# Optimization experiments

Measured on AMD Instinct MI355X. Metric: run time of the kernel, lower is better.

The kernel has to match this reference:

```python
import jax, jax.numpy as jnp
import numpy as np

KSIZE = 3; STRIDE = 1; RATE = 2; FUSE_K = 3; SCALE = 10.0; EPS = 1e-4
B, C, RH, RW = 2, 128, 80, 80  # raw (full-res) feature shape


def setup_inputs() -> dict:
    key = jax.random.key(0)
    ks = jax.random.split(key, 5)
    shp = (B, C, RH, RW)
    names = ["left", "right", "mid", "raw_left", "raw_right"]
    return {n: jax.random.normal(k, shp, dtype=jnp.float32) for n, k in zip(names, ks)}


def _same_pads(H, W, k, s):
    oh, ow = -(-H // s), -(-W // s)
    ph = max(0, (oh - 1) * s + k - H)
    pw = max(0, (ow - 1) * s + k - W)
    return ((ph // 2, ph - ph // 2), (pw // 2, pw - pw // 2))


def extract_patches(x, k, s):
    # torch extract_image_patches with 'same' padding -> (b, L, c, k, k)
    b, c, H, W = x.shape
    pads = _same_pads(H, W, k, s)
    p = jax.lax.conv_general_dilated_patches(x, (k, k), (s, s), pads)  # (b, c*k*k, oh, ow)
    oh, ow = p.shape[2], p.shape[3]
    p = p.reshape(b, c, k, k, oh * ow)  # feature dim is channel-major (c, k, k), like torch unfold
    return p.transpose(0, 4, 1, 2, 3)


def _fuse(s, Hl, Wl, Hm, Wm):
    # diagonal fuse-conv: conv of (b,1,L,P) score image with eye(k), twice with transposes
    b = s.shape[0]
    k = FUSE_K
    eye = jnp.eye(k, dtype=s.dtype).reshape(1, 1, k, k)
    pad = ((k // 2, k // 2), (k // 2, k // 2))
    conv = lambda x: jax.lax.conv_general_dilated(x, eye, (1, 1), pad)
    x = conv(s.reshape(b, 1, Hl * Wl, Hm * Wm))
    x = x.reshape(b, Hl, Wl, Hm, Wm).transpose(0, 2, 1, 4, 3).reshape(b, 1, Wl * Hl, Wm * Hm)
    x = conv(x)
    x = x.reshape(b, Wl, Hl, Wm, Hm).transpose(0, 2, 1, 4, 3)  # (b, Hl, Wl, Hm, Wm)
    return x.reshape(b, Hl * Wl, Hm, Wm)


def _deconv_one(attn, patches):
    # torch conv_transpose2d(attn, patches, stride=RATE, padding=1):
    # conv with lhs dilation RATE, spatially-flipped kernel, padding k-1-1
    kk = patches.shape[-1]
    rhs = jnp.flip(patches, (-2, -1)).transpose(1, 0, 2, 3)  # (C, L, kk, kk)
    p = kk - 1 - 1
    out = jax.lax.conv_general_dilated(attn[None], rhs, (1, 1), ((p, p), (p, p)),
                                       lhs_dilation=(RATE, RATE),
                                       dimension_numbers=('NCHW', 'OIHW', 'NCHW'))
    return out[0]


def _forward(left, right, mid, raw_left, raw_right):
    kernel = 2 * RATE
    rawp_l = extract_patches(raw_left, kernel, RATE * STRIDE)   # (B, L, C, 4, 4)
    rawp_r = extract_patches(raw_right, kernel, RATE * STRIDE)
    # nearest downsample by rate
    l = left[:, :, ::RATE, ::RATE]
    r = right[:, :, ::RATE, ::RATE]
    m = mid[:, :, ::RATE, ::RATE]
    Hl, Wl = l.shape[2], l.shape[3]
    Hm, Wm = m.shape[2], m.shape[3]
    lp = extract_patches(l, KSIZE, STRIDE)   # (B, L, C, 3, 3)
    rp = extract_patches(r, KSIZE, STRIDE)
    mp = extract_patches(m, KSIZE, STRIDE)   # (B, P, C, 3, 3); conv2d(same-padded xi, w) == patch dot

    def norm(p):
        # torch: sqrt(reduce_sum(p^2 + eps)) -- eps added elementwise before the sum
        return p / jnp.sqrt(jnp.sum(p * p + EPS, axis=(2, 3, 4), keepdims=True))

    sl = jnp.einsum('bqcij,bpcij->bqp', norm(lp), mp).reshape(-1, Hl * Wl, Hm, Wm)
    sr = jnp.einsum('bqcij,bpcij->bqp', norm(rp), mp).reshape(-1, Hl * Wl, Hm, Wm)
    sl = _fuse(sl, Hl, Wl, Hm, Wm)
    sr = _fuse(sr, Hl, Wl, Hm, Wm)
    al = jax.nn.softmax(sl * SCALE, axis=1)
    ar = jax.nn.softmax(sr * SCALE, axis=1)
    y_l = jax.vmap(_deconv_one)(al, rawp_l) / 4.0   # (B, C, RH, RW)
    y_r = jax.vmap(_deconv_one)(ar, rawp_r) / 4.0
    # cos_function_weight: cosine blending ramp along width (1 at left edge -> 0 at right edge)
    w = 0.5 * (1.0 + jnp.cos(jnp.pi * jnp.arange(RW, dtype=y_l.dtype) / (RW - 1)))
    w = w.reshape(1, 1, 1, RW)
    return w * y_l + jnp.flip(w, 3) * y_r


def reference(left, right, mid, raw_left, raw_right):
    return _forward(left, right, mid, raw_left, raw_right)
```

## Files before the change

kernel.cpp:

```cpp
#include <hip/hip_runtime.h>
#include <hip/hip_bf16.h>

typedef __hip_bfloat16 bf16;
typedef __attribute__((ext_vector_type(8))) short short8;
typedef __attribute__((ext_vector_type(4))) float f32x4;
typedef float f32x4u __attribute__((ext_vector_type(4), aligned(4)));
typedef unsigned short ushort_t;

#define PI_F 3.14159265358979323846f
#define GPAD_Z 3111696L

#define GLOAD_LDS16(gp, lp)                                                    \
  __builtin_amdgcn_global_load_lds(                                            \
      (const __attribute__((address_space(1))) unsigned int*)(gp),             \
      (__attribute__((address_space(3))) unsigned int*)(lp), 16, 0, 0)

__global__ __launch_bounds__(128) void prep_pt(const float* __restrict__ left,
                                               const float* __restrict__ right,
                                               const float* __restrict__ mid,
                                               bf16* __restrict__ PTe,
                                               bf16* __restrict__ MTe,
                                               float* __restrict__ SQ) {
  int q = blockIdx.x;
  int y = blockIdx.y;
  int c = threadIdx.x;
  int qi = q / 40, qj = q - qi * 40;
  const float* src;
  bf16* dst;
  int b;
  bool aside = (y < 4);
  if (aside) {
    b = y & 1;
    src = (y < 2) ? left : right;
    dst = PTe + (long)y * 1664 * 384;
  } else {
    b = y - 4;
    src = mid;
    dst = MTe + (long)(y - 4) * 1664 * 384;
  }
  float v = src[(((long)b * 128 + c) * 80 + 2 * qi) * 80 + 2 * qj];
  bf16 hi = __float2bfloat16(v);
  bf16 lo = __float2bfloat16(v - __bfloat162float(hi));
  if (aside) {
    dst[(long)q * 384 + c] = hi;
    dst[(long)q * 384 + 128 + c] = lo;
    dst[(long)q * 384 + 256 + c] = hi;
  } else {
    dst[(long)q * 384 + c] = hi;
    dst[(long)q * 384 + 128 + c] = hi;
    dst[(long)q * 384 + 256 + c] = lo;
  }
  if (aside) {
    __shared__ float red[128];
    red[c] = v * v;
    __syncthreads();
    for (int s = 64; s > 0; s >>= 1) {
      if (c < s) red[c] += red[c + s];
      __syncthreads();
    }
    if (c == 0) SQ[y * 1600 + q] = red[0];
  }
}

__global__ void invn_kernel(const float* __restrict__ SQ, float* __restrict__ INV) {
  int idx = blockIdx.x * 256 + threadIdx.x;
  if (idx >= 6400) return;
  int z = idx / 1600, q = idx - z * 1600;
  int qi = q / 40, qj = q - qi * 40;
  float s = 0.1152f;
  #pragma unroll
  for (int di = -1; di <= 1; ++di)
    #pragma unroll
    for (int dj = -1; dj <= 1; ++dj) {
      int a = qi + di, b = qj + dj;
      if (a >= 0 && a < 40 && b >= 0 && b < 40) s += SQ[z * 1600 + a * 40 + b];
    }
  INV[idx] = rsqrtf(s);
}

__global__ __launch_bounds__(256) void padzero_kernel(float* __restrict__ Gp) {
  int row = blockIdx.x;
  int z = blockIdx.y;
  float* R = Gp + (long)z * GPAD_Z + (long)row * 1764;
  int r42 = row % 42;
  if (r42 == 0 || r42 == 41) {
    for (int c = threadIdx.x; c < 1764; c += 256) R[c] = 0.f;
  } else {
    for (int i = threadIdx.x; i < 84; i += 256) {
      int c = (i >> 1) * 42 + ((i & 1) ? 41 : 0);
      R[c] = 0.f;
    }
  }
}

__global__ __launch_bounds__(256) void gemm_nt(const bf16* __restrict__ A,
                                               const bf16* __restrict__ B,
                                               float* __restrict__ C,
                                               int M, int N, int K,
                                               long Az, long Bz, long Cz,
                                               int bmod, int cpad) {
  int z = blockIdx.z;
  A += (long)z * Az;
  B += (long)(bmod ? (z & 1) : z) * Bz;
  C += (long)z * Cz;
  __shared__ bf16 As[128 * 32];
  __shared__ bf16 Bs[128 * 32];
  int lane = threadIdx.x & 63;
  int w = threadIdx.x >> 6;
  int mb = blockIdx.x * 128;
  int nb = blockIdx.y * 128;
  int lr = lane >> 2;
  int gb = (lane & 3) ^ ((lane >> 3) & 3);
  int lm = lane & 15;
  int swz = (lm >> 1) & 3;
  int kb = lane >> 4;
  int pos = (kb ^ swz) * 8;
  int warow = (w >> 1) * 64;
  int wbrow = (w & 1) * 64;
  f32x4 acc[4][4];
  #pragma unroll
  for (int i = 0; i < 4; ++i)
    #pragma unroll
    for (int j = 0; j < 4; ++j) {
      f32x4 zv = {0.f, 0.f, 0.f, 0.f};
      acc[i][j] = zv;
    }
  for (int k0 = 0; k0 < K; k0 += 32) {
    __syncthreads();
    #pragma unroll
    for (int t = 0; t < 2; ++t) {
      int r = (w * 2 + t) * 16 + lr;
      GLOAD_LDS16(A + (long)(mb + r) * K + k0 + gb * 8, As + (w * 2 + t) * 512);
      GLOAD_LDS16(B + (long)(nb + r) * K + k0 + gb * 8, Bs + (w * 2 + t) * 512);
    }
    __syncthreads();
    short8 af[4], bfr[4];
    #pragma unroll
    for (int i = 0; i < 4; ++i) {
      af[i]  = *reinterpret_cast<const short8*>(As + (warow + i * 16 + lm) * 32 + pos);
      bfr[i] = *reinterpret_cast<const short8*>(Bs + (wbrow + i * 16 + lm) * 32 + pos);
    }
    #pragma unroll
    for (int i = 0; i < 4; ++i)
      #pragma unroll
      for (int j = 0; j < 4; ++j)
        acc[i][j] = __builtin_amdgcn_mfma_f32_16x16x32_bf16(af[i], bfr[j], acc[i][j], 0, 0, 0);
  }
  int m0 = mb + warow;
  int n0 = nb + wbrow;
  int col = lane & 15;
  int r0 = (lane >> 4) * 4;
  #pragma unroll
  for (int i = 0; i < 4; ++i)
    #pragma unroll
    for (int j = 0; j < 4; ++j) {
      int n = n0 + j * 16 + col;
      if (n < N) {
        int nc = cpad ? ((n / 40) * 42 + (n - (n / 40) * 40) + 43) : n;
        #pragma unroll
        for (int r = 0; r < 4; ++r) {
          int m = m0 + i * 16 + r0 + r;
          if (m < M) {
            long mr = cpad ? ((long)((m / 40) * 42 + (m - (m / 40) * 40) + 43) * 1764)
                           : ((long)m * N);
            C[mr + nc] = acc[i][j][r];
          }
        }
      }
    }
}

#define BAR() __builtin_amdgcn_s_barrier()
#define LGKM0() asm volatile("s_waitcnt lgkmcnt(0)" ::: "memory")
#define STAGE_A(tt, h)                                                         \
  { long _k = (long)(tt) * 64;                                                 \
    char* _d = lds + (((tt) & 1) << 16) + (((h) * 8 + w) << 11);               \
    GLOAD_LDS16(a_row[h] + _k, _d);                                            \
    GLOAD_LDS16(a_row[h] + _k + 32, _d + 1024); }
#define STAGE_B(tt, h)                                                         \
  { long _k = (long)(tt) * 64;                                                 \
    char* _d = lds + (((tt) & 1) << 16) + 32768 + (((h) * 8 + w) << 11);       \
    GLOAD_LDS16(b_row[h] + _k, _d);                                            \
    GLOAD_LDS16(b_row[h] + _k + 32, _d + 1024); }
#define LD8(off) (*reinterpret_cast<const short8*>(lds + (off)))
#define LOAD_A(bufo, mh)                                                       \
  { _Pragma("unroll") for (int i = 0; i < 4; ++i)                              \
      { _Pragma("unroll") for (int kc = 0; kc < 2; ++kc)                       \
          a[i][kc] = LD8((bufo) + (((wm * 8 + (mh) * 4 + i) * 2 + kc) << 10) + rd_off); } }
#define LOAD_B(dst, bufo, nh)                                                  \
  { _Pragma("unroll") for (int j = 0; j < 2; ++j)                              \
      { _Pragma("unroll") for (int kc = 0; kc < 2; ++kc)                       \
          dst[j][kc] = LD8((bufo) + 32768 + (((wn * 4 + (nh) * 2 + j) * 2 + kc) << 10) + rd_off); } }
#define MFMA16(mh, nh, bset)                                                   \
  { _Pragma("unroll") for (int kc = 0; kc < 2; ++kc)                           \
      { _Pragma("unroll") for (int i = 0; i < 4; ++i)                          \
          { _Pragma("unroll") for (int j = 0; j < 2; ++j)                      \
              acc[(mh) * 4 + i][(nh) * 2 + j] = __builtin_amdgcn_mfma_f32_16x16x32_bf16( \
                  a[i][kc], bset[j][kc], acc[(mh) * 4 + i][(nh) * 2 + j], 0, 0, 0); } } }

__global__ __launch_bounds__(512, 2) void gemm256_nt(const bf16* __restrict__ A,
                                                     const bf16* __restrict__ B,
                                                     float* __restrict__ C,
                                                     int M, int N, int K,
                                                     long Az, long Bz, long Cz,
                                                     int nballoc) {
  __shared__ __align__(16) char lds[131072];
  int z = blockIdx.z;
  A += (long)z * Az;
  B += (long)z * Bz;
  C += (long)z * Cz;
  int tid = threadIdx.x;
  int lane = tid & 63;
  int w = tid >> 6;
  int wm = w >> 2;
  int wn = w & 3;
  int mb = blockIdx.x * 256;
  int nb = blockIdx.y * 256;
  int NT = K >> 6;

  int srcb = (lane << 4) ^ (lane & 32);
  int r_src = srcb >> 6;
  int c_src = (srcb & 63) >> 1;
  const bf16* a_row[2];
  const bf16* b_row[2];
  #pragma unroll
  for (int h = 0; h < 2; ++h) {
    a_row[h] = A + (long)(mb + (h * 8 + w) * 16 + r_src) * K + c_src;
    int br = nb + (h * 8 + w) * 16 + r_src;
    if (br > nballoc - 1) br = nballoc - 1;
    b_row[h] = B + (long)br * K + c_src;
  }
  int rd_off = (((lane & 15) << 6) | ((lane >> 4) << 4)) ^ ((lane & 8) << 2);

  short8 a[4][2], p0[2][2], p1[2][2];
  f32x4 acc[8][4];
  #pragma unroll
  for (int i = 0; i < 8; ++i)
    #pragma unroll
    for (int j = 0; j < 4; ++j) {
      f32x4 zv = {0.f, 0.f, 0.f, 0.f};
      acc[i][j] = zv;
    }

  STAGE_A(0, 0); STAGE_A(0, 1); STAGE_B(0, 0); STAGE_B(0, 1);
  STAGE_A(1, 0); STAGE_A(1, 1); STAGE_B(1, 0);
  asm volatile("s_waitcnt vmcnt(6)" ::: "memory");
  BAR();

  for (int t = 0; t < NT; ++t) {
    int bufo = (t & 1) << 16;
    LOAD_A(bufo, 0);
    LOAD_B(p0, bufo, 0);
    if (t + 1 < NT) STAGE_B(t + 1, 1);
    BAR(); LGKM0();
    __builtin_amdgcn_s_setprio(1); MFMA16(0, 0, p0); __builtin_amdgcn_s_setprio(0);
    BAR();
    LOAD_B(p1, bufo, 1);
    BAR(); LGKM0();
    __builtin_amdgcn_s_setprio(1); MFMA16(0, 1, p1); __builtin_amdgcn_s_setprio(0);
    BAR();
    LOAD_A(bufo, 1);
    BAR(); LGKM0();
    __builtin_amdgcn_s_setprio(1); MFMA16(1, 1, p1); __builtin_amdgcn_s_setprio(0);
    BAR();
    LOAD_B(p0, bufo, 0);
    BAR(); LGKM0();
    __builtin_amdgcn_s_setprio(1); MFMA16(1, 0, p0); __builtin_amdgcn_s_setprio(0);
    BAR();
    if (t + 2 < NT) {
      STAGE_A(t + 2, 0); STAGE_A(t + 2, 1); STAGE_B(t + 2, 0);
      asm volatile("s_waitcnt vmcnt(6)" ::: "memory");
      BAR();
    } else if (t + 1 < NT) {
      asm volatile("s_waitcnt vmcnt(0)" ::: "memory");
      BAR();
    }
  }

  int col = lane & 15;
  int r0 = (lane >> 4) * 4;
  int m_base = mb + wm * 128;
  int n_base = nb + wn * 64;
  #pragma unroll
  for (int i = 0; i < 8; ++i)
    #pragma unroll
    for (int j = 0; j < 4; ++j) {
      int n = n_base + j * 16 + col;
      if (n < N) {
        #pragma unroll
        for (int r = 0; r < 4; ++r) {
          int m = m_base + i * 16 + r0 + r;
          C[(long)m * N + n] = acc[i][j][r];
        }
      }
    }
}

__device__ __forceinline__ float ps9(const float* __restrict__ Gz, int q2, int p2) {
  int qi2 = q2 / 40, qj2 = q2 - qi2 * 40;
  int pi2 = p2 / 40, pj2 = p2 - pi2 * 40;
  const float* base = Gz + (long)(qi2 * 42 + qj2 + 43) * 1764 + (pi2 * 42 + pj2 + 43);
  float t = 0.f;
  #pragma unroll
  for (int di = -1; di <= 1; ++di)
    #pragma unroll
    for (int dj = -1; dj <= 1; ++dj)
      t += base[(long)(di * 42 + dj) * 1765];
  return t;
}

__global__ __launch_bounds__(256) void s1fuse1_kernel(const float* __restrict__ Gp,
                                                      const float* __restrict__ INV,
                                                      float* __restrict__ S2) {
  int b = blockIdx.x;
  int x = b & 7;
  int j = b >> 3;
  int half = (j >= 625) ? 1 : 0;
  int chunk = x + 8 * half;
  int z = chunk >> 2;
  int qq = chunk & 3;
  int s_local = j - half * 625;
  unsigned int gid = (unsigned int)s_local * 256u + threadIdx.x;
  int q_local = gid / 400u;
  int quad = gid - q_local * 400u;
  int q = qq * 400 + q_local;
  int p0 = quad * 4;
  int qi = q / 40, qj = q - qi * 40;
  int pi = p0 / 40, pj0 = p0 - pi * 40;
  const float* Gz = Gp + (long)z * GPAD_Z;
  const float* IVz = INV + z * 1600;
  float* Srow = S2 + ((long)z * 1600 + q) * 1600 + p0;

  if (qj >= 1 && qj <= 38) {
    long R0C0 = (long)(qi * 42 + qj + 43) * 1764 + (pi * 42 + pj0 + 43);
    f32x4 cs[5];
    #pragma unroll
    for (int s = 0; s < 5; ++s) {
      const float* pb = Gz + R0C0 + (long)(s - 2) * 1765;
      f32x4 a0 = *(const f32x4u*)(pb - 42 * 1765);
      f32x4 a1 = *(const f32x4u*)(pb);
      f32x4 a2 = *(const f32x4u*)(pb + 42 * 1765);
      cs[s] = a0 + a1 + a2;
    }
    f32x4 c12 = cs[1] + cs[2];
    f32x4 c23 = cs[2] + cs[3];
    f32x4 psm = cs[0] + c12;
    f32x4 ps0 = c12 + cs[3];
    f32x4 psp = c23 + cs[4];
    if (pj0 == 0) {
      int p2 = p0 - 1;
      psm[0] = (p2 >= 0) ? ps9(Gz, q - 1, p2) : 0.f;
    } else if (pj0 == 36) {
      int p2 = p0 + 4;
      psp[3] = (p2 < 1600) ? ps9(Gz, q + 1, p2) : 0.f;
    }
    float wm = IVz[q - 1], w0 = IVz[q], wp = IVz[q + 1];
    f32x4 outv = psm * wm + ps0 * w0 + psp * wp;
    *reinterpret_cast<f32x4*>(Srow) = outv;
  } else {
    f32x4 outv;
    #pragma unroll
    for (int t = 0; t < 4; ++t) {
      int p = p0 + t;
      float s = 0.f;
      #pragma unroll
      for (int d = -1; d <= 1; ++d) {
        int q2 = q + d, p2 = p + d;
        bool ok = ((unsigned)q2 < 1600u) && ((unsigned)p2 < 1600u);
        if (ok) s += IVz[q2] * ps9(Gz, q2, p2);
      }
      outv[t] = s;
    }
    *reinterpret_cast<f32x4*>(Srow) = outv;
  }
}

__global__ __launch_bounds__(256) void fuse2_kernel(const float* __restrict__ S2,
                                                    float* __restrict__ S3) {
  int z = blockIdx.y;
  int bx = blockIdx.x;
  int xc = bx & 7, rest = bx >> 3;
  int lid = (xc < 4 ? xc * 313 : 1252 + (xc - 4) * 312) + rest;
  unsigned int gid = (unsigned int)lid * 256u + threadIdx.x;
  int q = gid / 400u;
  int quad = gid - q * 400u;
  int p0 = quad * 4;
  const float* S = S2 + (long)z * 2560000;
  int il = q / 40, jl = q - il * 40;
  int im = p0 / 40, jm = p0 - im * 40;
  int u = jl * 40 + il;
  f32x4 acc = {0.f, 0.f, 0.f, 0.f};
  #pragma unroll
  for (int d = -1; d <= 1; ++d) {
    int u2 = u + d;
    if ((unsigned)u2 >= 1600u) continue;
    int q2 = (u2 % 40) * 40 + u2 / 40;
    int imd = im + d;
    if ((unsigned)imd < 40u) {
      acc += *reinterpret_cast<const f32x4*>(S + (long)q2 * 1600 + imd * 40 + jm);
    } else {
      #pragma unroll
      for (int t = 0; t < 4; ++t) {
        int v2 = (jm + t) * 40 + im + d;
        if ((unsigned)v2 < 1600u) {
          int p2 = (v2 % 40) * 40 + v2 / 40;
          acc[t] += S[(long)q2 * 1600 + p2];
        }
      }
    }
  }
  *reinterpret_cast<f32x4*>(S3 + ((long)z * 1600 + q) * 1600 + p0) = acc;
}

__global__ __launch_bounds__(256) void smax_part(const float* __restrict__ S3,
                                                 float* __restrict__ Pm,
                                                 float* __restrict__ Ps) {
  int z = blockIdx.z, qc = blockIdx.y;
  int pl = threadIdx.x & 63;
  int ql = threadIdx.x >> 6;
  int p = blockIdx.x * 64 + pl;
  const float* S = S3 + (long)z * 2560000;
  float m = -1e30f, s = 0.f;
  for (int i = 0; i < 50; ++i) {
    int q = qc * 200 + i * 4 + ql;
    float x = 10.f * S[(long)q * 1600 + p];
    if (x > m) { s *= __expf(m - x); m = x; }
    s += __expf(x - m);
  }
  __shared__ float lm[4][64], ls[4][64];
  lm[ql][pl] = m;
  ls[ql][pl] = s;
  __syncthreads();
  if (ql == 0) {
    float M = m, SS = s;
    #pragma unroll
    for (int j = 1; j < 4; ++j) {
      float mj = lm[j][pl], sj = ls[j][pl];
      if (mj > M) { SS = SS * __expf(M - mj) + sj; M = mj; }
      else SS += sj * __expf(mj - M);
    }
    Pm[((long)z * 8 + qc) * 1600 + p] = M;
    Ps[((long)z * 8 + qc) * 1600 + p] = SS;
  }
}

__global__ __launch_bounds__(256) void smax_write(const float* __restrict__ S3,
                                                  const float* __restrict__ Pm,
                                                  const float* __restrict__ Ps,
                                                  bf16* __restrict__ AT) {
  int z = blockIdx.z;
  int p0 = blockIdx.x * 64, q0 = blockIdx.y * 64;
  int pl = threadIdx.x & 63, ql = threadIdx.x >> 6;
  __shared__ float lfm[64], lfs[64];
  if (ql == 0) {
    int p = p0 + pl;
    float M = -1e30f;
    #pragma unroll
    for (int c = 0; c < 8; ++c) M = fmaxf(M, Pm[((long)z * 8 + c) * 1600 + p]);
    float S = 0.f;
    #pragma unroll
    for (int c = 0; c < 8; ++c)
      S += Ps[((long)z * 8 + c) * 1600 + p] * __expf(Pm[((long)z * 8 + c) * 1600 + p] - M);
    lfm[pl] = M;
    lfs[pl] = 1.f / S;
  }
  __syncthreads();
  __shared__ ushort_t T[64][66];
  float fm = lfm[pl];
  float fs = lfs[pl];
  const float* S = S3 + (long)z * 2560000;
  #pragma unroll
  for (int i = 0; i < 16; ++i) {
    int qq = ql + i * 4;
    float x = 10.f * S[(long)(q0 + qq) * 1600 + p0 + pl];
    bf16 h = __float2bfloat16(__expf(x - fm) * fs);
    T[pl][qq] = *reinterpret_cast<ushort_t*>(&h);
  }
  __syncthreads();
  int rp = threadIdx.x >> 5;
  int j = threadIdx.x & 31;
  #pragma unroll
  for (int pass = 0; pass < 8; ++pass) {
    int row = pass * 8 + rp;
    unsigned int vv = (unsigned int)T[row][2 * j] | ((unsigned int)T[row][2 * j + 1] << 16);
    *reinterpret_cast<unsigned int*>(AT + ((long)z * 1664 + p0 + row) * 1600 + q0 + 2 * j) = vv;
  }
}

__global__ __launch_bounds__(256) void rawpt_kernel(const float* __restrict__ rawL,
                                                    const float* __restrict__ rawR,
                                                    bf16* __restrict__ RAWPT) {
  int z = blockIdx.z;
  int r = blockIdx.y * 4 + (threadIdx.x >> 6);
  int q = blockIdx.x * 64 + (threadIdx.x & 63);
  const float* raw = ((z < 2) ? rawL : rawR) + (long)(z & 1) * 819200;
  int c = r >> 4, i = (r >> 2) & 3, j = r & 3;
  int qi = q / 40, qj = q - qi * 40;
  int y = 2 * qi + i - 1, x = 2 * qj + j - 1;
  float v = 0.f;
  if (y >= 0 && y < 80 && x >= 0 && x < 80) v = raw[((long)c * 80 + y) * 80 + x];
  RAWPT[((long)z * 2048 + r) * 1600 + q] = __float2bfloat16(v);
}

__global__ __launch_bounds__(256) void paste_kernel(const float* __restrict__ Z,
                                                    float* __restrict__ out) {
  int t8 = blockIdx.x * 256 + threadIdx.x;
  int g = t8 % 10;
  int r = t8 / 10;
  int x0 = g * 8;
  int h = x0 >> 1;
  int y = r % 80;
  int cc = (r / 80) % 128;
  int b = r / (80 * 128);
  int imA = (y - 1) >> 1, ipA = y - 2 * imA + 1;
  const long zs = 2048L * 1600;
  const float* ZL = Z + (long)b * zs;
  const float* ZR = Z + (long)(2 + b) * zs;
  f32x4 EL = {0.f,0.f,0.f,0.f}, OL = {0.f,0.f,0.f,0.f};
  f32x4 ER = {0.f,0.f,0.f,0.f}, OR_ = {0.f,0.f,0.f,0.f};
  #pragma unroll
  for (int a = 0; a < 2; ++a) {
    int im = imA + a;
    if ((unsigned)im > 39u) continue;
    int ip = ipA - 2 * a;
    long rb = (long)(cc * 16 + ip * 4) * 1600 + im * 40;
    f32x4 l3 = *(const f32x4u*)(ZL + rb + 3 * 1600 + h - 1);
    f32x4 l1 = *(const f32x4u*)(ZL + rb + 1 * 1600 + h);
    f32x4 l2 = *(const f32x4u*)(ZL + rb + 2 * 1600 + h);
    f32x4 l0 = *(const f32x4u*)(ZL + rb + 0 * 1600 + h + 1);
    f32x4 r3 = *(const f32x4u*)(ZR + rb + 3 * 1600 + h - 1);
    f32x4 r1 = *(const f32x4u*)(ZR + rb + 1 * 1600 + h);
    f32x4 r2 = *(const f32x4u*)(ZR + rb + 2 * 1600 + h);
    f32x4 r0 = *(const f32x4u*)(ZR + rb + 0 * 1600 + h + 1);
    if (x0 == 0) { l3[0] = 0.f; r3[0] = 0.f; }
    if (x0 == 72) { l0[3] = 0.f; r0[3] = 0.f; }
    EL += l3 + l1; OL += l2 + l0;
    ER += r3 + r1; OR_ += r2 + r0;
  }
  f32x4 o0, o1;
  #pragma unroll
  for (int k = 0; k < 4; ++k) {
    int xe = x0 + 2 * k, xo = xe + 1;
    float ce = cosf(PI_F * xe / 79.f);
    float co = cosf(PI_F * xo / 79.f);
    float ve = 0.25f * (0.5f * (1.f + ce) * EL[k] + 0.5f * (1.f - ce) * ER[k]);
    float vo = 0.25f * (0.5f * (1.f + co) * OL[k] + 0.5f * (1.f - co) * OR_[k]);
    if (k < 2) { o0[2 * k] = ve; o0[2 * k + 1] = vo; }
    else { o1[2 * (k - 2)] = ve; o1[2 * (k - 2) + 1] = vo; }
  }
  float* dst = out + (long)r * 80 + x0;
  *reinterpret_cast<f32x4*>(dst) = o0;
  *reinterpret_cast<f32x4*>(dst + 4) = o1;
}

extern "C" void kernel_launch(void* const* d_in, const int* in_sizes, int n_in,
                              void* d_out, int out_size, void* d_ws, size_t ws_size,
                              hipStream_t stream) {
  const float* left  = (const float*)d_in[0];
  const float* right = (const float*)d_in[1];
  const float* mid   = (const float*)d_in[2];
  const float* rawL  = (const float*)d_in[3];
  const float* rawR  = (const float*)d_in[4];
  float* out = (float*)d_out;
  char* ws = (char*)d_ws;

  bf16*  PTe   = (bf16*)(ws + 0);
  bf16*  MTe   = (bf16*)(ws + 5111808);
  float* SQ    = (float*)(ws + 7667712);
  float* INV   = (float*)(ws + 7693312);
  float* Pm    = (float*)(ws + 7718912);
  float* Ps    = (float*)(ws + 7923712);
  float* X     = (float*)(ws + 8179712);
  float* Y     = (float*)(ws + 60608512);
  bf16*  AT    = (bf16*)(ws + 101568512);
  bf16*  RAWPT = (bf16*)Y;

  prep_pt<<<dim3(1600, 6, 1), 128, 0, stream>>>(left, right, mid, PTe, MTe, SQ);
  invn_kernel<<<25, 256, 0, stream>>>(SQ, INV);
  padzero_kernel<<<dim3(1764, 4), 256, 0, stream>>>(X);
  gemm_nt<<<dim3(13, 13, 4), 256, 0, stream>>>(PTe, MTe, X, 1600, 1600, 384,
                                               1664L * 384, 1664L * 384, GPAD_Z, 1, 1);
  s1fuse1_kernel<<<10000, 256, 0, stream>>>(X, INV, Y);
  fuse2_kernel<<<dim3(2500, 4), 256, 0, stream>>>(Y, X);
  smax_part<<<dim3(25, 8, 4), 256, 0, stream>>>(X, Pm, Ps);
  smax_write<<<dim3(25, 25, 4), 256, 0, stream>>>(X, Pm, Ps, AT);
  rawpt_kernel<<<dim3(25, 512, 4), 256, 0, stream>>>(rawL, rawR, RAWPT);
  gemm256_nt<<<dim3(8, 7, 4), 512, 0, stream>>>(RAWPT, AT, X, 2048, 1600, 1600,
                                                2048L * 1600, 1664L * 1600, 2048L * 1600, 1664);
  paste_kernel<<<800, 256, 0, stream>>>(X, out);
}
```

Before: 310.0 us.

## Tile first fuse pass through LDS and remap gemm256 block order

The first diagonal-fuse kernel now stages row-summed triples of the padded score grid in shared memory per (qi, half-row, column chunk) tile. Each output then reads its 5 horizontal partial sums from LDS instead of issuing 15 strided global vector loads. Boundary query columns (qj 0 and 39) move to a separate small kernel that uses the old scalar path. The deconv GEMM also remaps its linear block id so blocks in the same z and neighbouring M tiles are scheduled together, which should improve L2 locality. The costs are an extra launch, LDS-limited occupancy, and possible LDS bank conflicts from the unaligned scalar reads.

```diff
diff --git a/kernel.cpp b/kernel.cpp
--- a/kernel.cpp
+++ b/kernel.cpp
@@ -205,7 +205,12 @@
                                                      long Az, long Bz, long Cz,
                                                      int nballoc) {
   __shared__ __align__(16) char lds[131072];
-  int z = blockIdx.z;
+  int l = blockIdx.x + (blockIdx.y << 3) + blockIdx.z * 56;
+  int x = l & 7;
+  int j7 = l >> 3;
+  int z = x >> 1;
+  int mb = (((x & 1) << 2) + (j7 & 3)) * 256;
+  int nb = (j7 >> 2) * 256;
   A += (long)z * Az;
   B += (long)z * Bz;
   C += (long)z * Cz;
@@ -214,8 +219,6 @@
   int w = tid >> 6;
   int wm = w >> 2;
   int wn = w & 3;
-  int mb = blockIdx.x * 256;
-  int nb = blockIdx.y * 256;
   int NT = K >> 6;
 
   int srcb = (lane << 4) ^ (lane & 32);
@@ -309,70 +312,108 @@
   return t;
 }
 
-__global__ __launch_bounds__(256) void s1fuse1_kernel(const float* __restrict__ Gp,
-                                                      const float* __restrict__ INV,
-                                                      float* __restrict__ S2) {
+__global__ __launch_bounds__(256) void s1fuse1_fast(const float* __restrict__ Gp,
+                                                    const float* __restrict__ INV,
+                                                    float* __restrict__ S2) {
+  __shared__ float Hs[23][176];
+  __shared__ float IVs[21];
   int b = blockIdx.x;
-  int x = b & 7;
-  int j = b >> 3;
-  int half = (j >= 625) ? 1 : 0;
-  int chunk = x + 8 * half;
-  int z = chunk >> 2;
-  int qq = chunk & 3;
-  int s_local = j - half * 625;
-  unsigned int gid = (unsigned int)s_local * 256u + threadIdx.x;
-  int q_local = gid / 400u;
-  int quad = gid - q_local * 400u;
-  int q = qq * 400 + q_local;
-  int p0 = quad * 4;
-  int qi = q / 40, qj = q - qi * 40;
-  int pi = p0 / 40, pj0 = p0 - pi * 40;
+  int g = b % 10;
+  int half = (b / 10) & 1;
+  int qi = (b / 20) % 40;
+  int z = b / 800;
+  int qj0 = half ? 20 : 1;
+  int tau0 = qj0 - 2;
+  int colL = 168 * g + 39;
   const float* Gz = Gp + (long)z * GPAD_Z;
   const float* IVz = INV + z * 1600;
-  float* Srow = S2 + ((long)z * 1600 + q) * 1600 + p0;
-
-  if (qj >= 1 && qj <= 38) {
-    long R0C0 = (long)(qi * 42 + qj + 43) * 1764 + (pi * 42 + pj0 + 43);
-    f32x4 cs[5];
-    #pragma unroll
-    for (int s = 0; s < 5; ++s) {
-      const float* pb = Gz + R0C0 + (long)(s - 2) * 1765;
-      f32x4 a0 = *(const f32x4u*)(pb - 42 * 1765);
-      f32x4 a1 = *(const f32x4u*)(pb);
-      f32x4 a2 = *(const f32x4u*)(pb + 42 * 1765);
-      cs[s] = a0 + a1 + a2;
-    }
-    f32x4 c12 = cs[1] + cs[2];
-    f32x4 c23 = cs[2] + cs[3];
-    f32x4 psm = cs[0] + c12;
-    f32x4 ps0 = c12 + cs[3];
-    f32x4 psp = c23 + cs[4];
+  int tid = threadIdx.x;
+
+  for (int idx = tid; idx < 23 * 44; idx += 256) {
+    int row = idx / 44;
+    int cv = idx - row * 44;
+    int gr = qi * 42 + 43 + tau0 + row;
+    int gc = colL + 4 * cv;
+    const float* p1 = Gz + (long)gr * 1764 + gc;
+    f32x4 v = *(const f32x4u*)(p1 - 42 * 1765) + *(const f32x4u*)(p1)
+            + *(const f32x4u*)(p1 + 42 * 1765);
+    *reinterpret_cast<f32x4*>(&Hs[row][4 * cv]) = v;
+  }
+  if (tid < 21) IVs[tid] = IVz[qi * 40 + qj0 - 1 + tid];
+  __syncthreads();
+
+  for (int j = tid; j < 760; j += 256) {
+    int jq = j / 40;
+    int jp = j - jq * 40;
+    int pblk = jp / 10;
+    int pj0 = (jp - pblk * 10) * 4;
+    int C0loc = pblk * 42 + pj0 + 4;
+    int p0 = g * 160 + jp * 4;
+    int qj = qj0 + jq;
+    int q = qi * 40 + qj;
+    f32x4 hs[5];
+    #pragma unroll
+    for (int s2 = 0; s2 < 5; ++s2) {
+      int tr = jq + s2;
+      int cc = C0loc + s2 - 2;
+      f32x4 hv = {Hs[tr][cc], Hs[tr][cc + 1], Hs[tr][cc + 2], Hs[tr][cc + 3]};
+      hs[s2] = hv;
+    }
+    f32x4 c12 = hs[1] + hs[2];
+    f32x4 c23 = hs[2] + hs[3];
+    f32x4 psm = hs[0] + c12;
+    f32x4 ps0 = c12 + hs[3];
+    f32x4 psp = c23 + hs[4];
     if (pj0 == 0) {
-      int p2 = p0 - 1;
-      psm[0] = (p2 >= 0) ? ps9(Gz, q - 1, p2) : 0.f;
+      float pv = 0.f;
+      if (p0 >= 1) {
+        int C2 = pblk * 42 + 1;
+        #pragma unroll
+        for (int dj = -1; dj <= 1; ++dj) pv += Hs[jq + 1 + dj][C2 + dj];
+      }
+      psm[0] = pv;
     } else if (pj0 == 36) {
-      int p2 = p0 + 4;
-      psp[3] = (p2 < 1600) ? ps9(Gz, q + 1, p2) : 0.f;
-    }
-    float wm = IVz[q - 1], w0 = IVz[q], wp = IVz[q + 1];
+      float pv = 0.f;
+      if (p0 + 4 < 1600) {
+        int C2 = pblk * 42 + 46;
+        #pragma unroll
+        for (int dj = -1; dj <= 1; ++dj) pv += Hs[jq + 3 + dj][C2 + dj];
+      }
+      psp[3] = pv;
+    }
+    float wm = IVs[jq], w0 = IVs[jq + 1], wp = IVs[jq + 2];
     f32x4 outv = psm * wm + ps0 * w0 + psp * wp;
-    *reinterpret_cast<f32x4*>(Srow) = outv;
-  } else {
-    f32x4 outv;
-    #pragma unroll
-    for (int t = 0; t < 4; ++t) {
-      int p = p0 + t;
-      float s = 0.f;
-      #pragma unroll
-      for (int d = -1; d <= 1; ++d) {
-        int q2 = q + d, p2 = p + d;
-        bool ok = ((unsigned)q2 < 1600u) && ((unsigned)p2 < 1600u);
-        if (ok) s += IVz[q2] * ps9(Gz, q2, p2);
-      }
-      outv[t] = s;
-    }
-    *reinterpret_cast<f32x4*>(Srow) = outv;
-  }
+    *reinterpret_cast<f32x4*>(S2 + ((long)z * 1600 + q) * 1600 + p0) = outv;
+  }
+}
+
+__global__ __launch_bounds__(256) void s1fuse1_slow(const float* __restrict__ Gp,
+                                                    const float* __restrict__ INV,
+                                                    float* __restrict__ S2) {
+  int z = blockIdx.y;
+  unsigned int gid = blockIdx.x * 256u + threadIdx.x;
+  int qidx = gid / 400u;
+  int quad = gid - qidx * 400u;
+  int qi = qidx >> 1;
+  int qj = (qidx & 1) * 39;
+  int q = qi * 40 + qj;
+  int p0 = quad * 4;
+  const float* Gz = Gp + (long)z * GPAD_Z;
+  const float* IVz = INV + z * 1600;
+  f32x4 outv;
+  #pragma unroll
+  for (int t = 0; t < 4; ++t) {
+    int p = p0 + t;
+    float s = 0.f;
+    #pragma unroll
+    for (int d = -1; d <= 1; ++d) {
+      int q2 = q + d, p2 = p + d;
+      bool ok = ((unsigned)q2 < 1600u) && ((unsigned)p2 < 1600u);
+      if (ok) s += IVz[q2] * ps9(Gz, q2, p2);
+    }
+    outv[t] = s;
+  }
+  *reinterpret_cast<f32x4*>(S2 + ((long)z * 1600 + q) * 1600 + p0) = outv;
 }
 
 __global__ __launch_bounds__(256) void fuse2_kernel(const float* __restrict__ S2,
@@ -580,7 +621,8 @@
   padzero_kernel<<<dim3(1764, 4), 256, 0, stream>>>(X);
   gemm_nt<<<dim3(13, 13, 4), 256, 0, stream>>>(PTe, MTe, X, 1600, 1600, 384,
                                                1664L * 384, 1664L * 384, GPAD_Z, 1, 1);
-  s1fuse1_kernel<<<10000, 256, 0, stream>>>(X, INV, Y);
+  s1fuse1_fast<<<3200, 256, 0, stream>>>(X, INV, Y);
+  s1fuse1_slow<<<dim3(125, 4), 256, 0, stream>>>(X, INV, Y);
   fuse2_kernel<<<dim3(2500, 4), 256, 0, stream>>>(Y, X);
   smax_part<<<dim3(25, 8, 4), 256, 0, stream>>>(X, Pm, Ps);
   smax_write<<<dim3(25, 25, 4), 256, 0, stream>>>(X, Pm, Ps, AT);
```

Result: no change. 304.7 us (-1.7%).
